# Kernel optimization log

Measured on AMD Instinct MI355X. Metric: run time of the kernel, lower is better.

Reference implementation:

```python
import jax, jax.numpy as jnp
import numpy as np

N, C, H, W = 8, 256, 128, 128   # images, AE-error channels, feature map size
A = 3                            # anchors per location (3 aspect ratios)
G = 64                           # GT boxes per image
STRIDE = 8
ANCHOR_SIZE = 32.0
ASPECT_RATIOS = (0.5, 1.0, 2.0)
UNK_CLASS = 80
D = 64                           # density_dim


def make_anchors():
    # detectron2 DefaultAnchorGenerator: cell anchors + grid shifts, (H, W, A) order, A fastest
    r = jnp.asarray(ASPECT_RATIOS, jnp.float32)
    w = ANCHOR_SIZE / jnp.sqrt(r)
    h = ANCHOR_SIZE * jnp.sqrt(r)
    cell = jnp.stack([-w / 2, -h / 2, w / 2, h / 2], axis=1)          # [A,4]
    sx = jnp.arange(W, dtype=jnp.float32) * STRIDE
    sy = jnp.arange(H, dtype=jnp.float32) * STRIDE
    yy, xx = jnp.meshgrid(sy, sx, indexing='ij')
    shifts = jnp.stack([xx, yy, xx, yy], axis=-1).reshape(-1, 4)      # [H*W,4]
    return (shifts[:, None, :] + cell[None, :, :]).reshape(-1, 4)     # [H*W*A,4]


def pairwise_iou(boxes, anchors):
    # boxes [G,4], anchors [R,4] -> [G,R]
    area_b = (boxes[:, 2] - boxes[:, 0]) * (boxes[:, 3] - boxes[:, 1])
    area_a = (anchors[:, 2] - anchors[:, 0]) * (anchors[:, 3] - anchors[:, 1])
    lt = jnp.maximum(boxes[:, None, :2], anchors[None, :, :2])
    rb = jnp.minimum(boxes[:, None, 2:], anchors[None, :, 2:])
    wh = jnp.clip(rb - lt, 0.0)
    inter = wh[..., 0] * wh[..., 1]
    return inter / jnp.maximum(area_b[:, None] + area_a[None, :] - inter, 1e-9)


def setup_inputs() -> dict:
    key = jax.random.key(0)
    k = jax.random.split(key, 9)
    err = jax.random.normal(k[0], (N, C, H, W), jnp.float32)
    err_map = jax.random.normal(k[1], (N, 1, H, W), jnp.float32)
    cxy = jax.random.uniform(k[2], (N, G, 2), minval=0.0, maxval=float(H * STRIDE))
    wh = jax.random.uniform(k[3], (N, G, 2), minval=16.0, maxval=128.0)
    gt_boxes = jnp.concatenate([cxy - wh / 2, cxy + wh / 2], axis=-1)
    gt_classes = jax.random.randint(k[4], (N, G), 0, 81, dtype=jnp.int32)
    w1 = jax.random.normal(k[5], (1, D), jnp.float32) * 0.5
    b1 = jnp.zeros((D,), jnp.float32)
    w2 = jax.random.normal(k[6], (D, D // 2), jnp.float32) * (1.0 / np.sqrt(D))
    b2 = jnp.zeros((D // 2,), jnp.float32)
    w3 = jax.random.normal(k[7], (D // 2, 1), jnp.float32) * (1.0 / np.sqrt(D // 2))
    b3 = jnp.zeros((1,), jnp.float32)
    return dict(err=err, err_map=err_map, gt_boxes=gt_boxes, w1=w1, b1=b1,
                w2=w2, b2=b2, w3=w3, b3=b3, gt_classes=gt_classes)


def reference(err, err_map, gt_boxes, w1, b1, w2, b2, w3, b3, gt_classes):
    # loss_ae: mean of squared flattened per-anchor errors (mean is permutation invariant)
    loss_ae = jnp.mean(err ** 2)

    # density head on every error-map pixel: Linear(1,D)-ReLU-Linear(D,D/2)-ReLU-Linear(D/2,1)
    pix = err_map.transpose(0, 2, 3, 1).reshape(N, H * W)              # [N,M]
    hmid = jax.nn.relu(pix[..., None] * w1[0] + b1)                    # [N,M,D]
    hmid = jax.nn.relu(jnp.einsum('nmd,de->nme', hmid, w2) + b2)       # [N,M,D/2]
    p_unk = (jnp.einsum('nme,eo->nmo', hmid, w3) + b3)[..., 0]         # [N,M]

    # anchor matching (torch.no_grad in original)
    anchors = make_anchors()                                           # [R,4]

    def match_one(boxes_i, classes_i):
        iou = pairwise_iou(boxes_i, anchors)                           # [G,R]
        idxs = jnp.argmax(iou, axis=0)                                 # per-anchor best GT
        return classes_i[idxs]                                         # [R]

    matched_classes = jax.vmap(match_one)(jax.lax.stop_gradient(gt_boxes), gt_classes)
    unk = (matched_classes == UNK_CLASS)                               # [N,R]
    mask = jnp.any(unk.reshape(N, H * W, A), axis=2).astype(jnp.float32)  # [N,M]

    # BCE with logits, mean reduction (stable form)
    loss_density = jnp.mean(jnp.logaddexp(0.0, p_unk) - p_unk * mask)
    return jnp.stack([loss_ae, loss_density])
```

## Files before the change

### kernel.cpp

```cpp
#include <hip/hip_runtime.h>
#include <math.h>

#define NIMG 8
#define HDIM 128
#define WDIM 128
#define GNUM 64
#define DDIM 64
#define EDIM 32
#define UNK_CLASS 80
#define NBLK 4096
#define DBLK 512
#define AE_THREADS (NBLK*256)

__global__ __launch_bounds__(256) void fused_kernel(
    const float* __restrict__ err,
    const float* __restrict__ err_map,
    const float* __restrict__ gt_boxes,
    const float* __restrict__ w1,
    const float* __restrict__ b1,
    const float* __restrict__ w2,
    const float* __restrict__ b2,
    const float* __restrict__ w3,
    const float* __restrict__ b3,
    const int*   __restrict__ gt_classes,
    float* __restrict__ ws)
{
    const int t = threadIdx.x;
    const int b = blockIdx.x;

    __shared__ float4 sboxes[GNUM];
    __shared__ int    scls[GNUM];
    __shared__ float  sw1[DDIM], sb1[DDIM], sb2[EDIM], sw3[EDIM];
    __shared__ __align__(16) float sw2[DDIM*EDIM];
    __shared__ float redA[4], redD[4];

    const float4* __restrict__ e4 = (const float4*)err;
    const int gtid = (b << 8) | t;
    float4 v0 = e4[gtid + 0*AE_THREADS];
    float4 v1 = e4[gtid + 1*AE_THREADS];
    float4 v2 = e4[gtid + 2*AE_THREADS];
    float4 v3 = e4[gtid + 3*AE_THREADS];
    float4 v4 = e4[gtid + 4*AE_THREADS];
    float4 v5 = e4[gtid + 5*AE_THREADS];
    float4 v6 = e4[gtid + 6*AE_THREADS];
    float4 v7 = e4[gtid + 7*AE_THREADS];
    float s0, s1, s2, s3;
    s0 = v0.x*v0.x; s1 = v0.y*v0.y; s2 = v0.z*v0.z; s3 = v0.w*v0.w;
    s0 = fmaf(v1.x,v1.x,s0); s1 = fmaf(v1.y,v1.y,s1); s2 = fmaf(v1.z,v1.z,s2); s3 = fmaf(v1.w,v1.w,s3);
    s0 = fmaf(v2.x,v2.x,s0); s1 = fmaf(v2.y,v2.y,s1); s2 = fmaf(v2.z,v2.z,s2); s3 = fmaf(v2.w,v2.w,s3);
    s0 = fmaf(v3.x,v3.x,s0); s1 = fmaf(v3.y,v3.y,s1); s2 = fmaf(v3.z,v3.z,s2); s3 = fmaf(v3.w,v3.w,s3);
    s0 = fmaf(v4.x,v4.x,s0); s1 = fmaf(v4.y,v4.y,s1); s2 = fmaf(v4.z,v4.z,s2); s3 = fmaf(v4.w,v4.w,s3);
    s0 = fmaf(v5.x,v5.x,s0); s1 = fmaf(v5.y,v5.y,s1); s2 = fmaf(v5.z,v5.z,s2); s3 = fmaf(v5.w,v5.w,s3);
    s0 = fmaf(v6.x,v6.x,s0); s1 = fmaf(v6.y,v6.y,s1); s2 = fmaf(v6.z,v6.z,s2); s3 = fmaf(v6.w,v6.w,s3);
    s0 = fmaf(v7.x,v7.x,s0); s1 = fmaf(v7.y,v7.y,s1); s2 = fmaf(v7.z,v7.z,s2); s3 = fmaf(v7.w,v7.w,s3);
    float aePart = (s0+s1) + (s2+s3);
    float dPart = 0.0f;

    if (b < DBLK) {
        const int n  = b >> 6;
        const int m  = ((b & 63) << 8) | t;

        if (t < GNUM)               sboxes[t]      = ((const float4*)gt_boxes)[n*GNUM + t];
        else if (t < 2*GNUM)        scls[t-GNUM]   = gt_classes[n*GNUM + (t-GNUM)];
        else if (t < 2*GNUM+DDIM) { sw1[t-128] = w1[t-128]; sb1[t-128] = b1[t-128]; }
        else if (t < 2*GNUM+DDIM+EDIM) { sb2[t-192] = b2[t-192]; sw3[t-192] = w3[t-192]; }
        for (int i = t; i < DDIM*EDIM; i += 256)
            sw2[i] = w2[i];
        __syncthreads();

        const float cx = (float)(m & (WDIM-1)) * 8.0f;
        const float cy = (float)(m >> 7) * 8.0f;
        const float s05 = sqrtf(0.5f), s2r = sqrtf(2.0f);
        const float hw0 = 0.5f*(32.0f/s05), hh0 = 0.5f*(32.0f*s05);
        const float hw1 = 16.0f,            hh1 = 16.0f;
        const float hw2 = 0.5f*(32.0f/s2r), hh2 = 0.5f*(32.0f*s2r);

        const float ax1[3] = {cx-hw0, cx-hw1, cx-hw2};
        const float ay1[3] = {cy-hh0, cy-hh1, cy-hh2};
        const float ax2[3] = {cx+hw0, cx+hw1, cx+hw2};
        const float ay2[3] = {cy+hh0, cy+hh1, cy+hh2};
        float areaA[3];
        #pragma unroll
        for (int a = 0; a < 3; ++a) areaA[a] = (ax2[a]-ax1[a])*(ay2[a]-ay1[a]);

        float bi[3] = {-1.f,-1.f,-1.f}, bd[3] = {1.f,1.f,1.f};
        int   idx[3] = {0,0,0};

        for (int g = 0; g < GNUM; ++g) {
            const float4 bx = sboxes[g];
            const float areaB = (bx.z-bx.x)*(bx.w-bx.y);
            #pragma unroll
            for (int a = 0; a < 3; ++a) {
                float lx = fmaxf(bx.x, ax1[a]), ly = fmaxf(bx.y, ay1[a]);
                float rx = fminf(bx.z, ax2[a]), ry = fminf(bx.w, ay2[a]);
                float iw = fmaxf(rx-lx, 0.f),   ih = fmaxf(ry-ly, 0.f);
                float inter = iw*ih;
                float dn = fmaxf(areaB + areaA[a] - inter, 1e-9f);
                if (inter*bd[a] > bi[a]*dn) { bi[a]=inter; bd[a]=dn; idx[a]=g; }
            }
        }
        const bool unk = (scls[idx[0]] == UNK_CLASS) |
                         (scls[idx[1]] == UNK_CLASS) |
                         (scls[idx[2]] == UNK_CLASS);
        const float mask = unk ? 1.0f : 0.0f;

        const float xv = err_map[(n << 14) + m];
        float acc[EDIM];
        #pragma unroll
        for (int e = 0; e < EDIM; ++e) acc[e] = sb2[e];

        const float4* __restrict__ sw2v = (const float4*)sw2;
        for (int d = 0; d < DDIM; ++d) {
            const float h = fmaxf(fmaf(xv, sw1[d], sb1[d]), 0.0f);
            #pragma unroll
            for (int j = 0; j < 8; ++j) {
                float4 wv = sw2v[(d << 3) + j];
                acc[4*j+0] = fmaf(h, wv.x, acc[4*j+0]);
                acc[4*j+1] = fmaf(h, wv.y, acc[4*j+1]);
                acc[4*j+2] = fmaf(h, wv.z, acc[4*j+2]);
                acc[4*j+3] = fmaf(h, wv.w, acc[4*j+3]);
            }
        }
        float p = b3[0];
        #pragma unroll
        for (int e = 0; e < EDIM; ++e)
            p = fmaf(fmaxf(acc[e], 0.0f), sw3[e], p);

        dPart = fmaxf(p, 0.0f) + log1pf(expf(-fabsf(p))) - p*mask;
    }

    float x = aePart, y = dPart;
    #pragma unroll
    for (int off = 32; off > 0; off >>= 1) {
        x += __shfl_xor(x, off, 64);
        y += __shfl_xor(y, off, 64);
    }
    if ((t & 63) == 0) { redA[t >> 6] = x; redD[t >> 6] = y; }
    __syncthreads();
    if (t == 0) {
        ws[b] = (redA[0]+redA[1]) + (redA[2]+redA[3]);
        if (b < DBLK) ws[NBLK + b] = (redD[0]+redD[1]) + (redD[2]+redD[3]);
    }
}

__global__ __launch_bounds__(256) void finalize_kernel(const float* __restrict__ ws,
                                                       float* __restrict__ out)
{
    const int t = threadIdx.x;
    float sa = 0.f, sd = 0.f;
    for (int i = t; i < NBLK; i += 256) sa += ws[i];
    for (int i = t; i < DBLK; i += 256) sd += ws[NBLK + i];
    #pragma unroll
    for (int off = 32; off > 0; off >>= 1) {
        sa += __shfl_xor(sa, off, 64);
        sd += __shfl_xor(sd, off, 64);
    }
    __shared__ float ra[4], rd[4];
    if ((t & 63) == 0) { ra[t >> 6] = sa; rd[t >> 6] = sd; }
    __syncthreads();
    if (t == 0) {
        out[0] = ((ra[0]+ra[1])+(ra[2]+ra[3])) * (1.0f/33554432.0f);
        out[1] = ((rd[0]+rd[1])+(rd[2]+rd[3])) * (1.0f/131072.0f);
    }
}

extern "C" void kernel_launch(void* const* d_in, const int* in_sizes, int n_in,
                              void* d_out, int out_size, void* d_ws, size_t ws_size,
                              hipStream_t stream) {
    const float* err        = (const float*)d_in[0];
    const float* err_map    = (const float*)d_in[1];
    const float* gt_boxes   = (const float*)d_in[2];
    const float* w1         = (const float*)d_in[3];
    const float* b1         = (const float*)d_in[4];
    const float* w2         = (const float*)d_in[5];
    const float* b2         = (const float*)d_in[6];
    const float* w3         = (const float*)d_in[7];
    const float* b3         = (const float*)d_in[8];
    const int*   gt_classes = (const int*)d_in[9];
    float* out = (float*)d_out;
    float* ws  = (float*)d_ws;

    fused_kernel<<<NBLK, 256, 0, stream>>>(err, err_map, gt_boxes, w1, b1, w2, b2,
                                           w3, b3, gt_classes, ws);
    finalize_kernel<<<1, 256, 0, stream>>>(ws, out);
}
```

Measured before the change: 214.3 us.

## Split density and AE-sum work into separate blocks, drop shared-memory staging

Instead of every block doing both the AE squared-sum chunk and (for the first 512) the density work, the grid now gives the first 512 blocks only density/anchor-matching work and 4096 additional blocks only the AE reduction, with contiguous per-block loads for the AE part. The density path reads boxes, classes and MLP weights straight from global memory (uniform loads, likely scalar/constant cache) instead of staging them into LDS with a barrier. This shortens the critical path of the slow density blocks and lets AE-only blocks stream freely, at the cost of more blocks and possible scalar-load latency in the inner loops.

```diff
diff --git a/kernel.cpp b/kernel.cpp
--- a/kernel.cpp
+++ b/kernel.cpp
@@ -1,16 +1,13 @@
 #include <hip/hip_runtime.h>
 #include <math.h>
 
-#define NIMG 8
-#define HDIM 128
-#define WDIM 128
 #define GNUM 64
 #define DDIM 64
 #define EDIM 32
 #define UNK_CLASS 80
-#define NBLK 4096
 #define DBLK 512
-#define AE_THREADS (NBLK*256)
+#define ABLK 4096
+#define NBLK (DBLK + ABLK)
 
 __global__ __launch_bounds__(256) void fused_kernel(
     const float* __restrict__ err,
@@ -27,48 +24,35 @@
 {
     const int t = threadIdx.x;
     const int b = blockIdx.x;
+    float part = 0.0f;
+    __shared__ float red[4];
 
-    __shared__ float4 sboxes[GNUM];
-    __shared__ int    scls[GNUM];
-    __shared__ float  sw1[DDIM], sb1[DDIM], sb2[EDIM], sw3[EDIM];
-    __shared__ __align__(16) float sw2[DDIM*EDIM];
-    __shared__ float redA[4], redD[4];
-
-    const float4* __restrict__ e4 = (const float4*)err;
-    const int gtid = (b << 8) | t;
-    float4 v0 = e4[gtid + 0*AE_THREADS];
-    float4 v1 = e4[gtid + 1*AE_THREADS];
-    float4 v2 = e4[gtid + 2*AE_THREADS];
-    float4 v3 = e4[gtid + 3*AE_THREADS];
-    float4 v4 = e4[gtid + 4*AE_THREADS];
-    float4 v5 = e4[gtid + 5*AE_THREADS];
-    float4 v6 = e4[gtid + 6*AE_THREADS];
-    float4 v7 = e4[gtid + 7*AE_THREADS];
-    float s0, s1, s2, s3;
-    s0 = v0.x*v0.x; s1 = v0.y*v0.y; s2 = v0.z*v0.z; s3 = v0.w*v0.w;
-    s0 = fmaf(v1.x,v1.x,s0); s1 = fmaf(v1.y,v1.y,s1); s2 = fmaf(v1.z,v1.z,s2); s3 = fmaf(v1.w,v1.w,s3);
-    s0 = fmaf(v2.x,v2.x,s0); s1 = fmaf(v2.y,v2.y,s1); s2 = fmaf(v2.z,v2.z,s2); s3 = fmaf(v2.w,v2.w,s3);
-    s0 = fmaf(v3.x,v3.x,s0); s1 = fmaf(v3.y,v3.y,s1); s2 = fmaf(v3.z,v3.z,s2); s3 = fmaf(v3.w,v3.w,s3);
-    s0 = fmaf(v4.x,v4.x,s0); s1 = fmaf(v4.y,v4.y,s1); s2 = fmaf(v4.z,v4.z,s2); s3 = fmaf(v4.w,v4.w,s3);
-    s0 = fmaf(v5.x,v5.x,s0); s1 = fmaf(v5.y,v5.y,s1); s2 = fmaf(v5.z,v5.z,s2); s3 = fmaf(v5.w,v5.w,s3);
-    s0 = fmaf(v6.x,v6.x,s0); s1 = fmaf(v6.y,v6.y,s1); s2 = fmaf(v6.z,v6.z,s2); s3 = fmaf(v6.w,v6.w,s3);
-    s0 = fmaf(v7.x,v7.x,s0); s1 = fmaf(v7.y,v7.y,s1); s2 = fmaf(v7.z,v7.z,s2); s3 = fmaf(v7.w,v7.w,s3);
-    float aePart = (s0+s1) + (s2+s3);
-    float dPart = 0.0f;
-
-    if (b < DBLK) {
+    if (b >= DBLK) {
+        const float4* __restrict__ e4 = (const float4*)err;
+        const int base = (b - DBLK) * 2048 + t;
+        float4 v0 = e4[base + 0*256];
+        float4 v1 = e4[base + 1*256];
+        float4 v2 = e4[base + 2*256];
+        float4 v3 = e4[base + 3*256];
+        float4 v4 = e4[base + 4*256];
+        float4 v5 = e4[base + 5*256];
+        float4 v6 = e4[base + 6*256];
+        float4 v7 = e4[base + 7*256];
+        float s0, s1, s2, s3;
+        s0 = v0.x*v0.x; s1 = v0.y*v0.y; s2 = v0.z*v0.z; s3 = v0.w*v0.w;
+        s0 = fmaf(v1.x,v1.x,s0); s1 = fmaf(v1.y,v1.y,s1); s2 = fmaf(v1.z,v1.z,s2); s3 = fmaf(v1.w,v1.w,s3);
+        s0 = fmaf(v2.x,v2.x,s0); s1 = fmaf(v2.y,v2.y,s1); s2 = fmaf(v2.z,v2.z,s2); s3 = fmaf(v2.w,v2.w,s3);
+        s0 = fmaf(v3.x,v3.x,s0); s1 = fmaf(v3.y,v3.y,s1); s2 = fmaf(v3.z,v3.z,s2); s3 = fmaf(v3.w,v3.w,s3);
+        s0 = fmaf(v4.x,v4.x,s0); s1 = fmaf(v4.y,v4.y,s1); s2 = fmaf(v4.z,v4.z,s2); s3 = fmaf(v4.w,v4.w,s3);
+        s0 = fmaf(v5.x,v5.x,s0); s1 = fmaf(v5.y,v5.y,s1); s2 = fmaf(v5.z,v5.z,s2); s3 = fmaf(v5.w,v5.w,s3);
+        s0 = fmaf(v6.x,v6.x,s0); s1 = fmaf(v6.y,v6.y,s1); s2 = fmaf(v6.z,v6.z,s2); s3 = fmaf(v6.w,v6.w,s3);
+        s0 = fmaf(v7.x,v7.x,s0); s1 = fmaf(v7.y,v7.y,s1); s2 = fmaf(v7.z,v7.z,s2); s3 = fmaf(v7.w,v7.w,s3);
+        part = (s0+s1) + (s2+s3);
+    } else {
         const int n  = b >> 6;
         const int m  = ((b & 63) << 8) | t;
 
-        if (t < GNUM)               sboxes[t]      = ((const float4*)gt_boxes)[n*GNUM + t];
-        else if (t < 2*GNUM)        scls[t-GNUM]   = gt_classes[n*GNUM + (t-GNUM)];
-        else if (t < 2*GNUM+DDIM) { sw1[t-128] = w1[t-128]; sb1[t-128] = b1[t-128]; }
-        else if (t < 2*GNUM+DDIM+EDIM) { sb2[t-192] = b2[t-192]; sw3[t-192] = w3[t-192]; }
-        for (int i = t; i < DDIM*EDIM; i += 256)
-            sw2[i] = w2[i];
-        __syncthreads();
-
-        const float cx = (float)(m & (WDIM-1)) * 8.0f;
+        const float cx = (float)(m & 127) * 8.0f;
         const float cy = (float)(m >> 7) * 8.0f;
         const float s05 = sqrtf(0.5f), s2r = sqrtf(2.0f);
         const float hw0 = 0.5f*(32.0f/s05), hh0 = 0.5f*(32.0f*s05);
@@ -86,77 +70,71 @@
         float bi[3] = {-1.f,-1.f,-1.f}, bd[3] = {1.f,1.f,1.f};
         int   idx[3] = {0,0,0};
 
+        const float* __restrict__ bp = gt_boxes + n*GNUM*4;
+        #pragma unroll 4
         for (int g = 0; g < GNUM; ++g) {
-            const float4 bx = sboxes[g];
-            const float areaB = (bx.z-bx.x)*(bx.w-bx.y);
+            const float bx1 = bp[4*g+0], by1 = bp[4*g+1];
+            const float bx2 = bp[4*g+2], by2 = bp[4*g+3];
+            const float areaB = (bx2-bx1)*(by2-by1);
             #pragma unroll
             for (int a = 0; a < 3; ++a) {
-                float lx = fmaxf(bx.x, ax1[a]), ly = fmaxf(bx.y, ay1[a]);
-                float rx = fminf(bx.z, ax2[a]), ry = fminf(bx.w, ay2[a]);
-                float iw = fmaxf(rx-lx, 0.f),   ih = fmaxf(ry-ly, 0.f);
+                float lx = fmaxf(bx1, ax1[a]), ly = fmaxf(by1, ay1[a]);
+                float rx = fminf(bx2, ax2[a]), ry = fminf(by2, ay2[a]);
+                float iw = fmaxf(rx-lx, 0.f),  ih = fmaxf(ry-ly, 0.f);
                 float inter = iw*ih;
                 float dn = fmaxf(areaB + areaA[a] - inter, 1e-9f);
                 if (inter*bd[a] > bi[a]*dn) { bi[a]=inter; bd[a]=dn; idx[a]=g; }
             }
         }
-        const bool unk = (scls[idx[0]] == UNK_CLASS) |
-                         (scls[idx[1]] == UNK_CLASS) |
-                         (scls[idx[2]] == UNK_CLASS);
+        const int* __restrict__ cp = gt_classes + n*GNUM;
+        const bool unk = (cp[idx[0]] == UNK_CLASS) |
+                         (cp[idx[1]] == UNK_CLASS) |
+                         (cp[idx[2]] == UNK_CLASS);
         const float mask = unk ? 1.0f : 0.0f;
 
         const float xv = err_map[(n << 14) + m];
         float acc[EDIM];
         #pragma unroll
-        for (int e = 0; e < EDIM; ++e) acc[e] = sb2[e];
+        for (int e = 0; e < EDIM; ++e) acc[e] = b2[e];
 
-        const float4* __restrict__ sw2v = (const float4*)sw2;
+        #pragma unroll 2
         for (int d = 0; d < DDIM; ++d) {
-            const float h = fmaxf(fmaf(xv, sw1[d], sb1[d]), 0.0f);
+            const float h = fmaxf(fmaf(xv, w1[d], b1[d]), 0.0f);
+            const float* __restrict__ wr = w2 + d*EDIM;
             #pragma unroll
-            for (int j = 0; j < 8; ++j) {
-                float4 wv = sw2v[(d << 3) + j];
-                acc[4*j+0] = fmaf(h, wv.x, acc[4*j+0]);
-                acc[4*j+1] = fmaf(h, wv.y, acc[4*j+1]);
-                acc[4*j+2] = fmaf(h, wv.z, acc[4*j+2]);
-                acc[4*j+3] = fmaf(h, wv.w, acc[4*j+3]);
-            }
+            for (int e = 0; e < EDIM; ++e)
+                acc[e] = fmaf(h, wr[e], acc[e]);
         }
         float p = b3[0];
         #pragma unroll
         for (int e = 0; e < EDIM; ++e)
-            p = fmaf(fmaxf(acc[e], 0.0f), sw3[e], p);
+            p = fmaf(fmaxf(acc[e], 0.0f), w3[e], p);
 
-        dPart = fmaxf(p, 0.0f) + log1pf(expf(-fabsf(p))) - p*mask;
+        part = fmaxf(p, 0.0f) + log1pf(expf(-fabsf(p))) - p*mask;
     }
 
-    float x = aePart, y = dPart;
+    float x = part;
     #pragma unroll
-    for (int off = 32; off > 0; off >>= 1) {
-        x += __shfl_xor(x, off, 64);
-        y += __shfl_xor(y, off, 64);
-    }
-    if ((t & 63) == 0) { redA[t >> 6] = x; redD[t >> 6] = y; }
+    for (int off = 32; off > 0; off >>= 1) x += __shfl_xor(x, off, 64);
+    if ((t & 63) == 0) red[t >> 6] = x;
     __syncthreads();
-    if (t == 0) {
-        ws[b] = (redA[0]+redA[1]) + (redA[2]+redA[3]);
-        if (b < DBLK) ws[NBLK + b] = (redD[0]+redD[1]) + (redD[2]+redD[3]);
-    }
+    if (t == 0) ws[b] = (red[0]+red[1]) + (red[2]+red[3]);
 }
 
 __global__ __launch_bounds__(256) void finalize_kernel(const float* __restrict__ ws,
                                                        float* __restrict__ out)
 {
     const int t = threadIdx.x;
-    float sa = 0.f, sd = 0.f;
-    for (int i = t; i < NBLK; i += 256) sa += ws[i];
-    for (int i = t; i < DBLK; i += 256) sd += ws[NBLK + i];
+    float sd = 0.f, sa = 0.f;
+    for (int i = t; i < DBLK; i += 256) sd += ws[i];
+    for (int i = DBLK + t; i < NBLK; i += 256) sa += ws[i];
     #pragma unroll
     for (int off = 32; off > 0; off >>= 1) {
+        sd += __shfl_xor(sd, off, 64);
         sa += __shfl_xor(sa, off, 64);
-        sd += __shfl_xor(sd, off, 64);
     }
-    __shared__ float ra[4], rd[4];
-    if ((t & 63) == 0) { ra[t >> 6] = sa; rd[t >> 6] = sd; }
+    __shared__ float rd[4], ra[4];
+    if ((t & 63) == 0) { rd[t >> 6] = sd; ra[t >> 6] = sa; }
     __syncthreads();
     if (t == 0) {
         out[0] = ((ra[0]+ra[1])+(ra[2]+ra[3])) * (1.0f/33554432.0f);
```

After: 222.0 us. +3.6%, slower.
